# Kernel tuning notes

Measured on AMD Instinct MI355X. Metric: run time of the kernel, lower is better.

## Reference

```python
import jax, jax.numpy as jnp
import numpy as np

DEPTH_CHANNELS = 64
OUT_CHANNELS = 128
IN_CHANNELS = 256
BEV_W, BEV_H = 432, 496  # interpolate target size (height=432, width=496 in torch's (H,W) order)


def setup_inputs() -> dict:
    key = jax.random.key(0)
    k1, k2 = jax.random.split(key)
    B, H, W = 4, 32, 88
    feat_2d = jax.random.normal(k1, (B, IN_CHANNELS, H, W), dtype=jnp.float32)
    # conv1x1 weight: (out=64+128, in=256), bias (192,)
    Wc = jax.random.normal(k2, (DEPTH_CHANNELS + OUT_CHANNELS, IN_CHANNELS), dtype=jnp.float32) * 0.02
    bc = jnp.zeros((DEPTH_CHANNELS + OUT_CHANNELS,), dtype=jnp.float32)
    return {"feat_2d": feat_2d, "Wc": Wc, "bc": bc}


def reference(feat_2d, Wc, bc):
    # 1x1 conv == channel GEMM
    x = jnp.einsum('bihw,oi->bohw', feat_2d, Wc) + bc[None, :, None, None]
    depth = jax.nn.softmax(x[:, :DEPTH_CHANNELS], axis=1)      # (B,64,H,W)
    context = x[:, DEPTH_CHANNELS:]                            # (B,C,H,W)
    # mean_d(context[c] * depth[d]) == context[c] * mean_d(depth)  (algebraically identical)
    bev = context * jnp.mean(depth, axis=1, keepdims=True)     # (B,C,H,W)
    # bilinear upsample, half-pixel convention == torch align_corners=False (upsampling)
    B, C = bev.shape[0], bev.shape[1]
    bev = jax.image.resize(bev, (B, C, BEV_W, BEV_H), method='bilinear')
    return bev
```

## Files before the change

### kernel.cpp

```cpp
#include <hip/hip_runtime.h>


#define K_IN    256
#define C_CTX   128
#define C_DEPTH 64
#define H_IN    32
#define W_IN    88
#define POS     (H_IN * W_IN)
#define H_OUT   432
#define W_OUT   496
#define XG      (W_OUT / 4)
#define GPP     (XG * H_OUT)
#define NPLANE  (4 * C_CTX)

#define KC      64
#define BPOS    64
#define LROW    68

__global__ __launch_bounds__(256) void conv1x1_kernel(
    const float* __restrict__ feat, const float* __restrict__ Wc,
    const float* __restrict__ bc, float* __restrict__ ctx)
{
    __shared__ float fs[BPOS * LROW];

    const int t       = threadIdx.x;
    const int posbase = blockIdx.x * BPOS;
    const int b       = blockIdx.z;
    const int wave    = __builtin_amdgcn_readfirstlane(t >> 6);
    const int cbase   = blockIdx.y * 64 + wave * 16;
    const int lane    = t & 63;

    const float* fb  = feat + (size_t)b * K_IN * POS + posbase;
    const int kl0 = t >> 4;
    const int p0  = (t & 15) * 4;

    float4 pre[4];
    #pragma unroll
    for (int j = 0; j < 4; ++j)
        pre[j] = *(const float4*)(fb + (size_t)(kl0 + 16 * j) * POS + p0);

    float acc[16];
    #pragma unroll
    for (int c = 0; c < 16; ++c) acc[c] = 0.f;

    const float* wbase = Wc + (size_t)(C_DEPTH + cbase) * K_IN;

    for (int kc = 0; kc < K_IN / KC; ++kc) {
        #pragma unroll
        for (int j = 0; j < 4; ++j) {
            int kl = kl0 + 16 * j;
            fs[(p0 + 0) * LROW + kl] = pre[j].x;
            fs[(p0 + 1) * LROW + kl] = pre[j].y;
            fs[(p0 + 2) * LROW + kl] = pre[j].z;
            fs[(p0 + 3) * LROW + kl] = pre[j].w;
        }
        __syncthreads();

        if (kc + 1 < K_IN / KC) {
            const float* fn = fb + (size_t)(kc + 1) * KC * POS;
            #pragma unroll
            for (int j = 0; j < 4; ++j)
                pre[j] = *(const float4*)(fn + (size_t)(kl0 + 16 * j) * POS + p0);
        }

        const float* wk = wbase + kc * KC;
        #pragma unroll
        for (int kk = 0; kk < KC; kk += 4) {
            float4 f = *(const float4*)&fs[lane * LROW + kk];
            #pragma unroll
            for (int c = 0; c < 16; ++c) {
                const float* w4 = wk + c * K_IN + kk;
                float a = acc[c];
                a = fmaf(f.x, w4[0], a);
                a = fmaf(f.y, w4[1], a);
                a = fmaf(f.z, w4[2], a);
                a = fmaf(f.w, w4[3], a);
                acc[c] = a;
            }
        }
        __syncthreads();
    }

    const float s = 1.0f / 64.0f;
    #pragma unroll
    for (int c = 0; c < 16; ++c) {
        float v = (acc[c] + bc[C_DEPTH + cbase + c]) * s;
        ctx[(size_t)(b * C_CTX + cbase + c) * POS + posbase + lane] = v;
    }
}

__global__ __launch_bounds__(256) void resize_kernel(
    const float* __restrict__ ctx, float* __restrict__ out)
{
    int g = blockIdx.x * blockDim.x + threadIdx.x;
    if (g >= GPP) return;
    int y  = g / XG;
    int xg = g - y * XG;
    int plane = blockIdx.y;

    const float* p = ctx + (size_t)plane * POS;

    const float SCY = 32.0f / 432.0f;
    const float SCX = 88.0f / 496.0f;

    float sy  = (y + 0.5f) * SCY - 0.5f;
    float fyf = floorf(sy);
    float wy  = sy - fyf;
    int y0  = (int)fyf;
    int y0c = max(y0, 0);
    int y1c = min(y0 + 1, H_IN - 1);
    const float* r0 = p + y0c * W_IN;
    const float* r1 = p + y1c * W_IN;

    float sx0 = (4 * xg + 0.5f) * SCX - 0.5f;
    int xb = (int)floorf(sx0);

    float ry[3];
    #pragma unroll
    for (int tp = 0; tp < 3; ++tp) {
        int xt = min(max(xb + tp, 0), W_IN - 1);
        float a = r0[xt];
        float b = r1[xt];
        ry[tp] = a + wy * (b - a);
    }

    float o[4];
    #pragma unroll
    for (int j = 0; j < 4; ++j) {
        float s  = (4 * xg + j + 0.5f) * SCX - 0.5f;
        float fs = floorf(s);
        float fx = s - fs;
        int tp = (int)fs - xb;
        o[j] = ry[tp] + fx * (ry[tp + 1] - ry[tp]);
    }

    size_t oidx = ((size_t)plane * H_OUT + y) * W_OUT + 4 * xg;
    float4 v = {o[0], o[1], o[2], o[3]};
    *(float4*)(out + oidx) = v;
}

extern "C" void kernel_launch(void* const* d_in, const int* in_sizes, int n_in,
                              void* d_out, int out_size, void* d_ws, size_t ws_size,
                              hipStream_t stream) {
    const float* feat = (const float*)d_in[0];
    const float* Wc   = (const float*)d_in[1];
    const float* bc   = (const float*)d_in[2];
    float* out = (float*)d_out;
    float* ctx = (float*)d_ws;

    dim3 b1(256);
    dim3 g1(POS / BPOS, C_CTX / 64, 4);
    conv1x1_kernel<<<g1, b1, 0, stream>>>(feat, Wc, bc, ctx);

    dim3 b2(256);
    dim3 g2((GPP + 255) / 256, NPLANE);
    resize_kernel<<<g2, b2, 0, stream>>>(ctx, out);
}
```

Measured before the change: 503.4 us.

## Retile conv1x1 as 4x4 register-blocked SMEM GEMM and use nontemporal resize stores

The conv kernel now stages both feature and weight tiles in shared memory and gives each thread a 4x4 outer-product block, where before it did scalar weight loads from global memory per FMA. The aim is to raise arithmetic intensity and remove redundant global weight traffic. The register prefetch of the next feature chunk is dropped, so loads and compute are no longer overlapped. The resize kernel's output writes become nontemporal stores, keeping the large streamed output out of the cache.

```diff
diff --git a/kernel.cpp b/kernel.cpp
--- a/kernel.cpp
+++ b/kernel.cpp
@@ -12,80 +12,89 @@
 #define XG      (W_OUT / 4)
 #define GPP     (XG * H_OUT)
 #define NPLANE  (4 * C_CTX)
+#define KC      64
 
-#define KC      64
-#define BPOS    64
-#define LROW    68
+typedef float f32x4 __attribute__((ext_vector_type(4)));
 
 __global__ __launch_bounds__(256) void conv1x1_kernel(
     const float* __restrict__ feat, const float* __restrict__ Wc,
     const float* __restrict__ bc, float* __restrict__ ctx)
 {
-    __shared__ float fs[BPOS * LROW];
+    __shared__ float As[KC * 64];
+    __shared__ float Bs[KC * 64];
 
     const int t       = threadIdx.x;
-    const int posbase = blockIdx.x * BPOS;
+    const int posbase = blockIdx.x * 64;
+    const int cbase   = blockIdx.y * 64;
     const int b       = blockIdx.z;
-    const int wave    = __builtin_amdgcn_readfirstlane(t >> 6);
-    const int cbase   = blockIdx.y * 64 + wave * 16;
-    const int lane    = t & 63;
 
-    const float* fb  = feat + (size_t)b * K_IN * POS + posbase;
-    const int kl0 = t >> 4;
-    const int p0  = (t & 15) * 4;
+    const int pg = t & 15;
+    const int cg = t >> 4;
 
-    float4 pre[4];
+    const float* fb = feat + (size_t)b * K_IN * POS + posbase;
+    const float* wb = Wc + (size_t)(C_DEPTH + cbase) * K_IN;
+
+    float acc[4][4];
     #pragma unroll
-    for (int j = 0; j < 4; ++j)
-        pre[j] = *(const float4*)(fb + (size_t)(kl0 + 16 * j) * POS + p0);
-
-    float acc[16];
-    #pragma unroll
-    for (int c = 0; c < 16; ++c) acc[c] = 0.f;
-
-    const float* wbase = Wc + (size_t)(C_DEPTH + cbase) * K_IN;
+    for (int i = 0; i < 4; ++i)
+        #pragma unroll
+        for (int j = 0; j < 4; ++j) acc[i][j] = 0.f;
 
     for (int kc = 0; kc < K_IN / KC; ++kc) {
         #pragma unroll
         for (int j = 0; j < 4; ++j) {
-            int kl = kl0 + 16 * j;
-            fs[(p0 + 0) * LROW + kl] = pre[j].x;
-            fs[(p0 + 1) * LROW + kl] = pre[j].y;
-            fs[(p0 + 2) * LROW + kl] = pre[j].z;
-            fs[(p0 + 3) * LROW + kl] = pre[j].w;
+            int k  = (t >> 4) + 16 * j;
+            int p4 = (t & 15) * 4;
+            *(float4*)&As[k * 64 + p4] =
+                *(const float4*)(fb + (size_t)(kc * KC + k) * POS + p4);
+        }
+        #pragma unroll
+        for (int j = 0; j < 4; ++j) {
+            int ch = t >> 2;
+            int k  = (t & 3) * 4 + 16 * j;
+            float4 w = *(const float4*)(wb + (size_t)ch * K_IN + kc * KC + k);
+            Bs[(k + 0) * 64 + ch] = w.x;
+            Bs[(k + 1) * 64 + ch] = w.y;
+            Bs[(k + 2) * 64 + ch] = w.z;
+            Bs[(k + 3) * 64 + ch] = w.w;
         }
         __syncthreads();
 
-        if (kc + 1 < K_IN / KC) {
-            const float* fn = fb + (size_t)(kc + 1) * KC * POS;
-            #pragma unroll
-            for (int j = 0; j < 4; ++j)
-                pre[j] = *(const float4*)(fn + (size_t)(kl0 + 16 * j) * POS + p0);
-        }
-
-        const float* wk = wbase + kc * KC;
-        #pragma unroll
-        for (int kk = 0; kk < KC; kk += 4) {
-            float4 f = *(const float4*)&fs[lane * LROW + kk];
-            #pragma unroll
-            for (int c = 0; c < 16; ++c) {
-                const float* w4 = wk + c * K_IN + kk;
-                float a = acc[c];
-                a = fmaf(f.x, w4[0], a);
-                a = fmaf(f.y, w4[1], a);
-                a = fmaf(f.z, w4[2], a);
-                a = fmaf(f.w, w4[3], a);
-                acc[c] = a;
-            }
+        #pragma unroll 8
+        for (int k = 0; k < KC; ++k) {
+            float4 a = *(const float4*)&As[k * 64 + pg * 4];
+            float4 w = *(const float4*)&Bs[k * 64 + cg * 4];
+            acc[0][0] = fmaf(a.x, w.x, acc[0][0]);
+            acc[1][0] = fmaf(a.y, w.x, acc[1][0]);
+            acc[2][0] = fmaf(a.z, w.x, acc[2][0]);
+            acc[3][0] = fmaf(a.w, w.x, acc[3][0]);
+            acc[0][1] = fmaf(a.x, w.y, acc[0][1]);
+            acc[1][1] = fmaf(a.y, w.y, acc[1][1]);
+            acc[2][1] = fmaf(a.z, w.y, acc[2][1]);
+            acc[3][1] = fmaf(a.w, w.y, acc[3][1]);
+            acc[0][2] = fmaf(a.x, w.z, acc[0][2]);
+            acc[1][2] = fmaf(a.y, w.z, acc[1][2]);
+            acc[2][2] = fmaf(a.z, w.z, acc[2][2]);
+            acc[3][2] = fmaf(a.w, w.z, acc[3][2]);
+            acc[0][3] = fmaf(a.x, w.w, acc[0][3]);
+            acc[1][3] = fmaf(a.y, w.w, acc[1][3]);
+            acc[2][3] = fmaf(a.z, w.w, acc[2][3]);
+            acc[3][3] = fmaf(a.w, w.w, acc[3][3]);
         }
         __syncthreads();
     }
 
     const float s = 1.0f / 64.0f;
     #pragma unroll
-    for (int c = 0; c < 16; ++c) {
-        float v = (acc[c] + bc[C_DEPTH + cbase + c]) * s;
-        ctx[(size_t)(b * C_CTX + cbase + c) * POS + posbase + lane] = v;
+    for (int j = 0; j < 4; ++j) {
+        int ch = cbase + 4 * cg + j;
+        float bb = bc[C_DEPTH + ch];
+        float4 r;
+        r.x = (acc[0][j] + bb) * s;
+        r.y = (acc[1][j] + bb) * s;
+        r.z = (acc[2][j] + bb) * s;
+        r.w = (acc[3][j] + bb) * s;
+        *(float4*)(ctx + (size_t)(b * C_CTX + ch) * POS + posbase + 4 * pg) = r;
     }
 }
 
@@ -135,8 +144,8 @@
     }
 
     size_t oidx = ((size_t)plane * H_OUT + y) * W_OUT + 4 * xg;
-    float4 v = {o[0], o[1], o[2], o[3]};
-    *(float4*)(out + oidx) = v;
+    f32x4 v = {o[0], o[1], o[2], o[3]};
+    __builtin_nontemporal_store(v, (f32x4*)(out + oidx));
 }
 
 extern "C" void kernel_launch(void* const* d_in, const int* in_sizes, int n_in,
@@ -149,7 +158,7 @@
     float* ctx = (float*)d_ws;
 
     dim3 b1(256);
-    dim3 g1(POS / BPOS, C_CTX / 64, 4);
+    dim3 g1(POS / 64, C_CTX / 64, 4);
     conv1x1_kernel<<<g1, b1, 0, stream>>>(feat, Wc, bc, ctx);
 
     dim3 b2(256);
```

New measurement: 452.0 us. 1.11x faster.
